# Kernel tuning notes

Hardware: AMD Instinct MI355X
Metric: run time of the kernel (lower is better)

Reference implementation:

```python
import jax, jax.numpy as jnp
import numpy as np

B, T, C = 8, 1024, 576
NH, NKV = 9, 3          # query heads, kv heads
HD = C // NH            # 64 head dim
KVC = C // NKV          # 192 kv proj width
N_REP = NH // NKV       # 3


def setup_inputs() -> dict:
    key = jax.random.key(0)
    ks = jax.random.split(key, 9)
    s = 0.02
    return {
        "x": jax.random.normal(ks[0], (B, T, C), jnp.float32),
        "Wq": jax.random.normal(ks[1], (C, C), jnp.float32) * s,
        "bq": jax.random.normal(ks[2], (C,), jnp.float32) * s,
        "Wk": jax.random.normal(ks[3], (C, KVC), jnp.float32) * s,
        "bk": jax.random.normal(ks[4], (KVC,), jnp.float32) * s,
        "Wv": jax.random.normal(ks[5], (C, KVC), jnp.float32) * s,
        "bv": jax.random.normal(ks[6], (KVC,), jnp.float32) * s,
        "Wo": jax.random.normal(ks[7], (C, C), jnp.float32) * s,
        "bo": jax.random.normal(ks[8], (C,), jnp.float32) * s,
    }


def reference(x, Wq, bq, Wk, bk, Wv, bv, Wo, bo):
    Bx, Tx, Cx = x.shape
    q = x @ Wq + bq                                # [B,T,C]
    k = x @ Wk + bk                                # [B,T,KVC]
    v = x @ Wv + bv
    # split heads: q -> [B,NH,T,HD]; k,v -> [B,NKV,T,HD]
    q = q.reshape(Bx, Tx, NH, HD).transpose(0, 2, 1, 3)
    k = k.reshape(Bx, Tx, NKV, HD).transpose(0, 2, 1, 3)
    v = v.reshape(Bx, Tx, NKV, HD).transpose(0, 2, 1, 3)
    # repeat_kv: [B,NKV,T,HD] -> [B,NKV*N_REP,T,HD]
    k = jnp.repeat(k, N_REP, axis=1)
    v = jnp.repeat(v, N_REP, axis=1)
    att = jnp.einsum("bhqd,bhkd->bhqk", q, k) * (1.0 / np.sqrt(HD))
    mask = jnp.tril(jnp.ones((Tx, Tx), bool))
    att = jnp.where(mask, att, -jnp.inf)
    att = jax.nn.softmax(att, axis=-1)
    y = jnp.einsum("bhqk,bhkd->bhqd", att, v)      # [B,NH,T,HD]
    y = y.transpose(0, 2, 1, 3).reshape(Bx, Tx, Cx)
    return y @ Wo + bo
```

## Files before the change

kernel.cpp:

```cpp
#include <hip/hip_runtime.h>
#include <hip/hip_bf16.h>
#include <math.h>

#define B_    8
#define T_    1024
#define C_    576
#define NH_   9
#define NKV_  3
#define HD_   64
#define KVC_  192
#define NREP_ 3
#define NQKV_ 960

typedef __attribute__((ext_vector_type(8))) short bf16x8;
typedef __attribute__((ext_vector_type(4))) float f32x4;
typedef __attribute__((ext_vector_type(4))) int i32x4;

#define MFMA_16x16x32(a, b, c) __builtin_amdgcn_mfma_f32_16x16x32_bf16((a), (b), (c), 0, 0, 0)

__device__ __forceinline__ ushort f2bf(float f) {
  __hip_bfloat16 h = __float2bfloat16(f);
  return *reinterpret_cast<const ushort*>(&h);
}

__device__ __forceinline__ int swz(int row, int col) {
  int byte = (row << 7) + (col << 1);
  return (byte ^ ((row & 7) << 4)) >> 1;
}

__device__ __forceinline__ i32x4 packrow(const float* src) {
  const float4 a = *reinterpret_cast<const float4*>(src);
  const float4 b = *reinterpret_cast<const float4*>(src + 4);
  union { ushort u[8]; i32x4 v; } t;
  t.u[0] = f2bf(a.x); t.u[1] = f2bf(a.y); t.u[2] = f2bf(a.z); t.u[3] = f2bf(a.w);
  t.u[4] = f2bf(b.x); t.u[5] = f2bf(b.y); t.u[6] = f2bf(b.z); t.u[7] = f2bf(b.w);
  return t.v;
}

__global__ __launch_bounds__(256) void convert_x_kernel(
    const float* __restrict__ x, ushort* __restrict__ xb) {
  const size_t idx = ((size_t)blockIdx.x * 256 + threadIdx.x) * 8;
  *reinterpret_cast<i32x4*>(xb + idx) = packrow(x + idx);
}

__global__ __launch_bounds__(256) void convert_w_kernel(
    const float* __restrict__ Wq, const float* __restrict__ Wk,
    const float* __restrict__ Wv, const float* __restrict__ Wo,
    const float* __restrict__ bq, const float* __restrict__ bk,
    const float* __restrict__ bv, const float* __restrict__ bo,
    ushort* __restrict__ wqkvT, ushort* __restrict__ woT, float* __restrict__ bcat) {
  const int n = blockIdx.x * 256 + threadIdx.x;
  const int k8 = blockIdx.y;
  const float* src; int ld; ushort* dst;
  if (n < 576)      { src = Wq + n;        ld = C_;  dst = wqkvT + (size_t)n * C_; }
  else if (n < 768) { src = Wk + (n - 576); ld = KVC_; dst = wqkvT + (size_t)n * C_; }
  else if (n < 960) { src = Wv + (n - 768); ld = KVC_; dst = wqkvT + (size_t)n * C_; }
  else              { src = Wo + (n - 960); ld = C_;  dst = woT + (size_t)(n - 960) * C_; }
  union { ushort u[8]; i32x4 v; } t;
  #pragma unroll
  for (int e = 0; e < 8; e++) t.u[e] = f2bf(src[(size_t)(k8 * 8 + e) * ld]);
  *reinterpret_cast<i32x4*>(dst + k8 * 8) = t.v;
  if (k8 == 0) {
    if (n < 576)      bcat[n] = bq[n];
    else if (n < 768) bcat[n] = bk[n - 576];
    else if (n < 960) bcat[n] = bv[n - 768];
    else              bcat[n] = bo[n - 960];
  }
}

template<bool OUT_BF16>
__global__ __launch_bounds__(256) void gemm_mfma_kernel(
    const ushort* __restrict__ A, const ushort* __restrict__ Bt,
    const float* __restrict__ bias, void* __restrict__ Cp,
    int M, int K, int N, int q_cols) {
  __shared__ ushort As[128 * 64];
  __shared__ ushort Bs[64 * 64];
  const int bm = blockIdx.y * 128, bn = blockIdx.x * 64;
  const int tid = threadIdx.x;
  const int wave = tid >> 6, lane = tid & 63;
  const int lg = lane >> 4, ll = lane & 15;
  const int wm = (wave >> 1) * 64, wn = (wave & 1) * 32;
  f32x4 acc[4][2] = {};

  for (int k0 = 0; k0 < K; k0 += 64) {
    #pragma unroll
    for (int i = 0; i < 4; i++) {
      int c = tid + i * 256;
      int row = c >> 3, colb = (c & 7) * 8;
      *reinterpret_cast<i32x4*>(&As[swz(row, colb)]) =
          *reinterpret_cast<const i32x4*>(A + (size_t)(bm + row) * K + k0 + colb);
    }
    #pragma unroll
    for (int i = 0; i < 2; i++) {
      int c = tid + i * 256;
      int row = c >> 3, colb = (c & 7) * 8;
      *reinterpret_cast<i32x4*>(&Bs[swz(row, colb)]) =
          *reinterpret_cast<const i32x4*>(Bt + (size_t)(bn + row) * K + k0 + colb);
    }
    __syncthreads();

    bf16x8 af[4][2], bfr[2][2];
    #pragma unroll
    for (int mt = 0; mt < 4; mt++) {
      af[mt][0] = *reinterpret_cast<const bf16x8*>(&As[swz(wm + mt * 16 + ll, lg * 8)]);
      af[mt][1] = *reinterpret_cast<const bf16x8*>(&As[swz(wm + mt * 16 + ll, 32 + lg * 8)]);
    }
    #pragma unroll
    for (int nt = 0; nt < 2; nt++) {
      bfr[nt][0] = *reinterpret_cast<const bf16x8*>(&Bs[swz(wn + nt * 16 + ll, lg * 8)]);
      bfr[nt][1] = *reinterpret_cast<const bf16x8*>(&Bs[swz(wn + nt * 16 + ll, 32 + lg * 8)]);
    }
    #pragma unroll
    for (int mt = 0; mt < 4; mt++) {
      #pragma unroll
      for (int nt = 0; nt < 2; nt++) {
        acc[mt][nt] = MFMA_16x16x32(af[mt][0], bfr[nt][0], acc[mt][nt]);
        acc[mt][nt] = MFMA_16x16x32(af[mt][1], bfr[nt][1], acc[mt][nt]);
      }
    }
    __syncthreads();
  }

  #pragma unroll
  for (int mt = 0; mt < 4; mt++) {
    #pragma unroll
    for (int nt = 0; nt < 2; nt++) {
      const int col = bn + wn + nt * 16 + ll;
      const float scale = (col < q_cols) ? 0.125f : 1.0f;
      #pragma unroll
      for (int r = 0; r < 4; r++) {
        const int row = bm + wm + mt * 16 + lg * 4 + r;
        const float val = (acc[mt][nt][r] + bias[col]) * scale;
        if (OUT_BF16) ((ushort*)Cp)[(size_t)row * N + col] = f2bf(val);
        else          ((float*)Cp)[(size_t)row * N + col] = val;
      }
    }
  }
}

__global__ __launch_bounds__(256) void attn_mfma_kernel(
    const ushort* __restrict__ qkv, ushort* __restrict__ y) {
  const int qt = 15 - blockIdx.z, h = blockIdx.x, b = blockIdx.y;
  const int kvh = h / NREP_;
  const int tid = threadIdx.x;
  const int wave = tid >> 6, lane = tid & 63;
  const int lg = lane >> 4, ll = lane & 15;
  const int w16 = wave << 4;
  const int qrow0 = qt << 6;
  const int nk = (qt + 2) >> 1;

  __shared__ ushort Ks[2][64 * 64];
  __shared__ ushort Vts[2][64 * 64];
  __shared__ ushort Ps[4][16 * 64];

  const int ksub = tid >> 7, ktt = tid & 127;
  const int kr = ktt >> 2, kcb = (ktt & 3) << 4;
  const int vkp = ktt & 31, vds = (ktt >> 5) << 4;

  const ushort* qrow = qkv + (size_t)(b * T_ + qrow0 + w16 + ll) * NQKV_ + h * HD_;
  const bf16x8 qa0 = *reinterpret_cast<const bf16x8*>(qrow + lg * 8);
  const bf16x8 qa1 = *reinterpret_cast<const bf16x8*>(qrow + 32 + lg * 8);

  f32x4 o[4] = {};
  float m_i = -INFINITY, l_i = 0.f;

  i32x4 kra, krb, krc, krd, va0, va1, vb0, vb1;
  {
    const size_t rb = (size_t)(b * T_);
    const ushort* ks0 = qkv + (rb + ksub * 64 + kr) * NQKV_ + 576 + kvh * HD_ + kcb;
    const ushort* ks1 = ks0 + (size_t)32 * NQKV_;
    kra = *reinterpret_cast<const i32x4*>(ks0);
    krb = *reinterpret_cast<const i32x4*>(ks0 + 8);
    krc = *reinterpret_cast<const i32x4*>(ks1);
    krd = *reinterpret_cast<const i32x4*>(ks1 + 8);
    const ushort* v0 = qkv + (rb + ksub * 64 + vkp * 2) * NQKV_ + 768 + kvh * HD_ + vds;
    const ushort* v1 = v0 + NQKV_;
    va0 = *reinterpret_cast<const i32x4*>(v0); va1 = *reinterpret_cast<const i32x4*>(v0 + 8);
    vb0 = *reinterpret_cast<const i32x4*>(v1); vb1 = *reinterpret_cast<const i32x4*>(v1 + 8);
  }
  {
    *reinterpret_cast<i32x4*>(&Ks[ksub][swz(kr, kcb)]) = kra;
    *reinterpret_cast<i32x4*>(&Ks[ksub][swz(kr, kcb + 8)]) = krb;
    *reinterpret_cast<i32x4*>(&Ks[ksub][swz(kr + 32, kcb)]) = krc;
    *reinterpret_cast<i32x4*>(&Ks[ksub][swz(kr + 32, kcb + 8)]) = krd;
    union { i32x4 v; ushort u[8]; } a0, a1, c0, c1;
    a0.v = va0; a1.v = va1; c0.v = vb0; c1.v = vb1;
    #pragma unroll
    for (int e = 0; e < 8; e++) {
      *reinterpret_cast<uint*>(&Vts[ksub][swz(vds + e, vkp * 2)]) =
          (uint)a0.u[e] | ((uint)c0.u[e] << 16);
      *reinterpret_cast<uint*>(&Vts[ksub][swz(vds + 8 + e, vkp * 2)]) =
          (uint)a1.u[e] | ((uint)c1.u[e] << 16);
    }
  }
  __syncthreads();

  #pragma unroll 1
  for (int kt = 0; kt < nk; kt++) {
    if (kt + 1 < nk) {
      const size_t rb = (size_t)(b * T_ + ((kt + 1) << 7));
      const ushort* ks0 = qkv + (rb + ksub * 64 + kr) * NQKV_ + 576 + kvh * HD_ + kcb;
      const ushort* ks1 = ks0 + (size_t)32 * NQKV_;
      kra = *reinterpret_cast<const i32x4*>(ks0);
      krb = *reinterpret_cast<const i32x4*>(ks0 + 8);
      krc = *reinterpret_cast<const i32x4*>(ks1);
      krd = *reinterpret_cast<const i32x4*>(ks1 + 8);
      const ushort* v0 = qkv + (rb + ksub * 64 + vkp * 2) * NQKV_ + 768 + kvh * HD_ + vds;
      const ushort* v1 = v0 + NQKV_;
      va0 = *reinterpret_cast<const i32x4*>(v0); va1 = *reinterpret_cast<const i32x4*>(v0 + 8);
      vb0 = *reinterpret_cast<const i32x4*>(v1); vb1 = *reinterpret_cast<const i32x4*>(v1 + 8);
    }

    f32x4 s[8];
    #pragma unroll
    for (int kc = 0; kc < 8; kc++) {
      const int sub = kc >> 2, kcl = kc & 3;
      const bf16x8 kb0 = *reinterpret_cast<const bf16x8*>(&Ks[sub][swz(kcl * 16 + ll, lg * 8)]);
      const bf16x8 kb1 = *reinterpret_cast<const bf16x8*>(&Ks[sub][swz(kcl * 16 + ll, 32 + lg * 8)]);
      f32x4 z = {};
      z = MFMA_16x16x32(kb0, qa0, z);
      s[kc] = MFMA_16x16x32(kb1, qa1, z);
    }

    if (kt == nk - 1) {
      const int qg = qrow0 + w16 + ll - (kt << 7);
      #pragma unroll
      for (int kc = 0; kc < 8; kc++)
        #pragma unroll
        for (int r = 0; r < 4; r++)
          if (kc * 16 + lg * 4 + r > qg) s[kc][r] = -INFINITY;
    }

    float t0 = s[0][0];
    #pragma unroll
    for (int kc = 0; kc < 8; kc++)
      #pragma unroll
      for (int r = 0; r < 4; r++) t0 = fmaxf(t0, s[kc][r]);
    t0 = fmaxf(t0, __shfl_xor(t0, 16));
    t0 = fmaxf(t0, __shfl_xor(t0, 32));
    if (!__all(t0 <= m_i + 8.f)) {
      const float mn = fmaxf(m_i, t0);
      const float al = __expf(m_i - mn);
      m_i = mn;
      l_i *= al;
      #pragma unroll
      for (int r = 0; r < 4; r++) {
        const float ar = __shfl(al, lg * 4 + r);
        o[0][r] *= ar; o[1][r] *= ar; o[2][r] *= ar; o[3][r] *= ar;
      }
    }

    float rs = 0.f;
    ushort* Pw = Ps[wave];
    #pragma unroll
    for (int sub = 0; sub < 2; sub++) {
      #pragma unroll
      for (int kcl = 0; kcl < 4; kcl++) {
        const int kc = sub * 4 + kcl;
        float p0 = __expf(s[kc][0] - m_i);
        float p1 = __expf(s[kc][1] - m_i);
        float p2 = __expf(s[kc][2] - m_i);
        float p3 = __expf(s[kc][3] - m_i);
        rs += (p0 + p1) + (p2 + p3);
        uint w01 = (uint)f2bf(p0) | ((uint)f2bf(p1) << 16);
        uint w23 = (uint)f2bf(p2) | ((uint)f2bf(p3) << 16);
        *reinterpret_cast<uint*>(&Pw[swz(ll, kcl * 16 + lg * 4)])     = w01;
        *reinterpret_cast<uint*>(&Pw[swz(ll, kcl * 16 + lg * 4 + 2)]) = w23;
      }
      #pragma unroll
      for (int khl = 0; khl < 2; khl++) {
        const bf16x8 pa = *reinterpret_cast<const bf16x8*>(&Pw[swz(ll, khl * 32 + lg * 8)]);
        #pragma unroll
        for (int d0 = 0; d0 < 4; d0++) {
          const bf16x8 vb = *reinterpret_cast<const bf16x8*>(&Vts[sub][swz(d0 * 16 + ll, khl * 32 + lg * 8)]);
          o[d0] = MFMA_16x16x32(pa, vb, o[d0]);
        }
      }
    }
    rs += __shfl_xor(rs, 16);
    rs += __shfl_xor(rs, 32);
    l_i += rs;

    if (kt + 1 < nk) {
      __syncthreads();
      *reinterpret_cast<i32x4*>(&Ks[ksub][swz(kr, kcb)]) = kra;
      *reinterpret_cast<i32x4*>(&Ks[ksub][swz(kr, kcb + 8)]) = krb;
      *reinterpret_cast<i32x4*>(&Ks[ksub][swz(kr + 32, kcb)]) = krc;
      *reinterpret_cast<i32x4*>(&Ks[ksub][swz(kr + 32, kcb + 8)]) = krd;
      union { i32x4 v; ushort u[8]; } a0, a1, c0, c1;
      a0.v = va0; a1.v = va1; c0.v = vb0; c1.v = vb1;
      #pragma unroll
      for (int e = 0; e < 8; e++) {
        *reinterpret_cast<uint*>(&Vts[ksub][swz(vds + e, vkp * 2)]) =
            (uint)a0.u[e] | ((uint)c0.u[e] << 16);
        *reinterpret_cast<uint*>(&Vts[ksub][swz(vds + 8 + e, vkp * 2)]) =
            (uint)a1.u[e] | ((uint)c1.u[e] << 16);
      }
      __syncthreads();
    }
  }

  #pragma unroll
  for (int r = 0; r < 4; r++) {
    const float lr = __shfl(l_i, lg * 4 + r);
    const float inv = 1.f / lr;
    ushort* yrow = y + (size_t)(b * T_ + qrow0 + w16 + lg * 4 + r) * C_ + h * HD_;
    #pragma unroll
    for (int d0 = 0; d0 < 4; d0++) {
      yrow[d0 * 16 + ll] = f2bf(o[d0][r] * inv);
    }
  }
}

extern "C" void kernel_launch(void* const* d_in, const int* in_sizes, int n_in,
                              void* d_out, int out_size, void* d_ws, size_t ws_size,
                              hipStream_t stream) {
  const float* x  = (const float*)d_in[0];
  const float* Wq = (const float*)d_in[1];
  const float* bq = (const float*)d_in[2];
  const float* Wk = (const float*)d_in[3];
  const float* bk = (const float*)d_in[4];
  const float* Wv = (const float*)d_in[5];
  const float* bv = (const float*)d_in[6];
  const float* Wo = (const float*)d_in[7];
  const float* bo = (const float*)d_in[8];
  float* out = (float*)d_out;

  const int M = B_ * T_;
  ushort* wqkvT = (ushort*)d_ws;
  ushort* woT   = wqkvT + (size_t)NQKV_ * C_;
  float*  bcat  = (float*)(woT + (size_t)C_ * C_);
  ushort* qkv   = (ushort*)(bcat + 1536);
  ushort* y     = qkv + (size_t)M * NQKV_;
  ushort* xb    = y + (size_t)M * C_;

  convert_w_kernel<<<dim3(6, 72), 256, 0, stream>>>(Wq, Wk, Wv, Wo, bq, bk, bv, bo,
                                                    wqkvT, woT, bcat);
  convert_x_kernel<<<dim3((M * C_) / (256 * 8)), 256, 0, stream>>>(x, xb);
  gemm_mfma_kernel<true><<<dim3(NQKV_ / 64, M / 128), 256, 0, stream>>>(
      xb, wqkvT, bcat, qkv, M, C_, NQKV_, 576);
  attn_mfma_kernel<<<dim3(NH_, B_, 16), 256, 0, stream>>>(qkv, y);
  gemm_mfma_kernel<false><<<dim3(C_ / 64, M / 128), 256, 0, stream>>>(
      y, woT, bcat + NQKV_, out, M, C_, C_, 0);
}
```

Before: 84.91 us.

## Double attention query tile per block and switch softmax to exp2

Each attention block now has 512 threads covering 128 query rows, not 256 threads covering 64, so every K/V tile staged in shared memory serves twice as many queries. The grid halves, and per-thread global load work for K/V staging halves. The 1/sqrt(d)*log2(e) factor is folded into the Q projection scale so the softmax can use exp2f, with the rescale threshold adjusted to match. The risks are fewer blocks for the causal load balance, worse load balance because the diagonal tile now masks a larger span, and heavier shared-memory and register pressure per block.

```diff
diff --git a/kernel.cpp b/kernel.cpp
--- a/kernel.cpp
+++ b/kernel.cpp
@@ -126,7 +126,7 @@
     #pragma unroll
     for (int nt = 0; nt < 2; nt++) {
       const int col = bn + wn + nt * 16 + ll;
-      const float scale = (col < q_cols) ? 0.125f : 1.0f;
+      const float scale = (col < q_cols) ? 0.18033688011112042f : 1.0f;
       #pragma unroll
       for (int r = 0; r < 4; r++) {
         const int row = bm + wm + mt * 16 + lg * 4 + r;
@@ -138,59 +138,52 @@
   }
 }
 
-__global__ __launch_bounds__(256) void attn_mfma_kernel(
+__global__ __launch_bounds__(512) void attn_mfma_kernel(
     const ushort* __restrict__ qkv, ushort* __restrict__ y) {
-  const int qt = 15 - blockIdx.z, h = blockIdx.x, b = blockIdx.y;
+  const int h = blockIdx.x, b = blockIdx.y;
+  const int qblk = 7 - blockIdx.z;
   const int kvh = h / NREP_;
   const int tid = threadIdx.x;
   const int wave = tid >> 6, lane = tid & 63;
   const int lg = lane >> 4, ll = lane & 15;
-  const int w16 = wave << 4;
-  const int qrow0 = qt << 6;
-  const int nk = (qt + 2) >> 1;
+  const int wtile = wave >> 2, w16 = (wave & 3) << 4;
+  const int qrow0 = qblk << 7;
+  const int nk = qblk + 1;
 
   __shared__ ushort Ks[2][64 * 64];
   __shared__ ushort Vts[2][64 * 64];
-  __shared__ ushort Ps[4][16 * 64];
-
-  const int ksub = tid >> 7, ktt = tid & 127;
-  const int kr = ktt >> 2, kcb = (ktt & 3) << 4;
-  const int vkp = ktt & 31, vds = (ktt >> 5) << 4;
-
-  const ushort* qrow = qkv + (size_t)(b * T_ + qrow0 + w16 + ll) * NQKV_ + h * HD_;
+  __shared__ ushort Ps[8][16 * 64];
+
+  const int ksub = tid >> 8, stt = tid & 255;
+  const int kr = stt >> 2, kcb = (stt & 3) << 4;
+  const int vkp = stt & 31, vds = (stt >> 5) << 3;
+
+  const int qg_row = qrow0 + wtile * 64 + w16 + ll;
+  const ushort* qrow = qkv + (size_t)(b * T_ + qg_row) * NQKV_ + h * HD_;
   const bf16x8 qa0 = *reinterpret_cast<const bf16x8*>(qrow + lg * 8);
   const bf16x8 qa1 = *reinterpret_cast<const bf16x8*>(qrow + 32 + lg * 8);
 
   f32x4 o[4] = {};
   float m_i = -INFINITY, l_i = 0.f;
 
-  i32x4 kra, krb, krc, krd, va0, va1, vb0, vb1;
+  i32x4 kra, krb, va, vb;
   {
     const size_t rb = (size_t)(b * T_);
     const ushort* ks0 = qkv + (rb + ksub * 64 + kr) * NQKV_ + 576 + kvh * HD_ + kcb;
-    const ushort* ks1 = ks0 + (size_t)32 * NQKV_;
     kra = *reinterpret_cast<const i32x4*>(ks0);
     krb = *reinterpret_cast<const i32x4*>(ks0 + 8);
-    krc = *reinterpret_cast<const i32x4*>(ks1);
-    krd = *reinterpret_cast<const i32x4*>(ks1 + 8);
     const ushort* v0 = qkv + (rb + ksub * 64 + vkp * 2) * NQKV_ + 768 + kvh * HD_ + vds;
-    const ushort* v1 = v0 + NQKV_;
-    va0 = *reinterpret_cast<const i32x4*>(v0); va1 = *reinterpret_cast<const i32x4*>(v0 + 8);
-    vb0 = *reinterpret_cast<const i32x4*>(v1); vb1 = *reinterpret_cast<const i32x4*>(v1 + 8);
+    va = *reinterpret_cast<const i32x4*>(v0);
+    vb = *reinterpret_cast<const i32x4*>(v0 + NQKV_);
   }
   {
     *reinterpret_cast<i32x4*>(&Ks[ksub][swz(kr, kcb)]) = kra;
     *reinterpret_cast<i32x4*>(&Ks[ksub][swz(kr, kcb + 8)]) = krb;
-    *reinterpret_cast<i32x4*>(&Ks[ksub][swz(kr + 32, kcb)]) = krc;
-    *reinterpret_cast<i32x4*>(&Ks[ksub][swz(kr + 32, kcb + 8)]) = krd;
-    union { i32x4 v; ushort u[8]; } a0, a1, c0, c1;
-    a0.v = va0; a1.v = va1; c0.v = vb0; c1.v = vb1;
+    union { i32x4 v; ushort u[8]; } a0, b0; a0.v = va; b0.v = vb;
     #pragma unroll
     for (int e = 0; e < 8; e++) {
       *reinterpret_cast<uint*>(&Vts[ksub][swz(vds + e, vkp * 2)]) =
-          (uint)a0.u[e] | ((uint)c0.u[e] << 16);
-      *reinterpret_cast<uint*>(&Vts[ksub][swz(vds + 8 + e, vkp * 2)]) =
-          (uint)a1.u[e] | ((uint)c1.u[e] << 16);
+          (uint)a0.u[e] | ((uint)b0.u[e] << 16);
     }
   }
   __syncthreads();
@@ -200,15 +193,11 @@
     if (kt + 1 < nk) {
       const size_t rb = (size_t)(b * T_ + ((kt + 1) << 7));
       const ushort* ks0 = qkv + (rb + ksub * 64 + kr) * NQKV_ + 576 + kvh * HD_ + kcb;
-      const ushort* ks1 = ks0 + (size_t)32 * NQKV_;
       kra = *reinterpret_cast<const i32x4*>(ks0);
       krb = *reinterpret_cast<const i32x4*>(ks0 + 8);
-      krc = *reinterpret_cast<const i32x4*>(ks1);
-      krd = *reinterpret_cast<const i32x4*>(ks1 + 8);
       const ushort* v0 = qkv + (rb + ksub * 64 + vkp * 2) * NQKV_ + 768 + kvh * HD_ + vds;
-      const ushort* v1 = v0 + NQKV_;
-      va0 = *reinterpret_cast<const i32x4*>(v0); va1 = *reinterpret_cast<const i32x4*>(v0 + 8);
-      vb0 = *reinterpret_cast<const i32x4*>(v1); vb1 = *reinterpret_cast<const i32x4*>(v1 + 8);
+      va = *reinterpret_cast<const i32x4*>(v0);
+      vb = *reinterpret_cast<const i32x4*>(v0 + NQKV_);
     }
 
     f32x4 s[8];
@@ -223,7 +212,7 @@
     }
 
     if (kt == nk - 1) {
-      const int qg = qrow0 + w16 + ll - (kt << 7);
+      const int qg = qg_row - (kt << 7);
       #pragma unroll
       for (int kc = 0; kc < 8; kc++)
         #pragma unroll
@@ -231,16 +220,17 @@
           if (kc * 16 + lg * 4 + r > qg) s[kc][r] = -INFINITY;
     }
 
-    float t0 = s[0][0];
+    float mA[8];
     #pragma unroll
     for (int kc = 0; kc < 8; kc++)
-      #pragma unroll
-      for (int r = 0; r < 4; r++) t0 = fmaxf(t0, s[kc][r]);
+      mA[kc] = fmaxf(fmaxf(s[kc][0], s[kc][1]), fmaxf(s[kc][2], s[kc][3]));
+    float t0 = fmaxf(fmaxf(fmaxf(mA[0], mA[1]), fmaxf(mA[2], mA[3])),
+                     fmaxf(fmaxf(mA[4], mA[5]), fmaxf(mA[6], mA[7])));
     t0 = fmaxf(t0, __shfl_xor(t0, 16));
     t0 = fmaxf(t0, __shfl_xor(t0, 32));
-    if (!__all(t0 <= m_i + 8.f)) {
+    if (!__all(t0 <= m_i + 11.5415603f)) {
       const float mn = fmaxf(m_i, t0);
-      const float al = __expf(m_i - mn);
+      const float al = exp2f(m_i - mn);
       m_i = mn;
       l_i *= al;
       #pragma unroll
@@ -250,33 +240,36 @@
       }
     }
 
-    float rs = 0.f;
+    float rsub[2];
     ushort* Pw = Ps[wave];
     #pragma unroll
     for (int sub = 0; sub < 2; sub++) {
+      float rk[4];
       #pragma unroll
       for (int kcl = 0; kcl < 4; kcl++) {
         const int kc = sub * 4 + kcl;
-        float p0 = __expf(s[kc][0] - m_i);
-        float p1 = __expf(s[kc][1] - m_i);
-        float p2 = __expf(s[kc][2] - m_i);
-        float p3 = __expf(s[kc][3] - m_i);
-        rs += (p0 + p1) + (p2 + p3);
+        float p0 = exp2f(s[kc][0] - m_i);
+        float p1 = exp2f(s[kc][1] - m_i);
+        float p2 = exp2f(s[kc][2] - m_i);
+        float p3 = exp2f(s[kc][3] - m_i);
+        rk[kcl] = (p0 + p1) + (p2 + p3);
         uint w01 = (uint)f2bf(p0) | ((uint)f2bf(p1) << 16);
         uint w23 = (uint)f2bf(p2) | ((uint)f2bf(p3) << 16);
         *reinterpret_cast<uint*>(&Pw[swz(ll, kcl * 16 + lg * 4)])     = w01;
         *reinterpret_cast<uint*>(&Pw[swz(ll, kcl * 16 + lg * 4 + 2)]) = w23;
       }
+      rsub[sub] = (rk[0] + rk[1]) + (rk[2] + rk[3]);
       #pragma unroll
       for (int khl = 0; khl < 2; khl++) {
         const bf16x8 pa = *reinterpret_cast<const bf16x8*>(&Pw[swz(ll, khl * 32 + lg * 8)]);
         #pragma unroll
         for (int d0 = 0; d0 < 4; d0++) {
-          const bf16x8 vb = *reinterpret_cast<const bf16x8*>(&Vts[sub][swz(d0 * 16 + ll, khl * 32 + lg * 8)]);
-          o[d0] = MFMA_16x16x32(pa, vb, o[d0]);
+          const bf16x8 vbr = *reinterpret_cast<const bf16x8*>(&Vts[sub][swz(d0 * 16 + ll, khl * 32 + lg * 8)]);
+          o[d0] = MFMA_16x16x32(pa, vbr, o[d0]);
         }
       }
     }
+    float rs = rsub[0] + rsub[1];
     rs += __shfl_xor(rs, 16);
     rs += __shfl_xor(rs, 32);
     l_i += rs;
@@ -285,16 +278,11 @@
       __syncthreads();
       *reinterpret_cast<i32x4*>(&Ks[ksub][swz(kr, kcb)]) = kra;
       *reinterpret_cast<i32x4*>(&Ks[ksub][swz(kr, kcb + 8)]) = krb;
-      *reinterpret_cast<i32x4*>(&Ks[ksub][swz(kr + 32, kcb)]) = krc;
-      *reinterpret_cast<i32x4*>(&Ks[ksub][swz(kr + 32, kcb + 8)]) = krd;
-      union { i32x4 v; ushort u[8]; } a0, a1, c0, c1;
-      a0.v = va0; a1.v = va1; c0.v = vb0; c1.v = vb1;
+      union { i32x4 v; ushort u[8]; } a0, b0; a0.v = va; b0.v = vb;
       #pragma unroll
       for (int e = 0; e < 8; e++) {
         *reinterpret_cast<uint*>(&Vts[ksub][swz(vds + e, vkp * 2)]) =
-            (uint)a0.u[e] | ((uint)c0.u[e] << 16);
-        *reinterpret_cast<uint*>(&Vts[ksub][swz(vds + 8 + e, vkp * 2)]) =
-            (uint)a1.u[e] | ((uint)c1.u[e] << 16);
+            (uint)a0.u[e] | ((uint)b0.u[e] << 16);
       }
       __syncthreads();
     }
@@ -304,7 +292,7 @@
   for (int r = 0; r < 4; r++) {
     const float lr = __shfl(l_i, lg * 4 + r);
     const float inv = 1.f / lr;
-    ushort* yrow = y + (size_t)(b * T_ + qrow0 + w16 + lg * 4 + r) * C_ + h * HD_;
+    ushort* yrow = y + (size_t)(b * T_ + qrow0 + wtile * 64 + w16 + lg * 4 + r) * C_ + h * HD_;
     #pragma unroll
     for (int d0 = 0; d0 < 4; d0++) {
       yrow[d0 * 16 + ll] = f2bf(o[d0][r] * inv);
@@ -339,7 +327,7 @@
   convert_x_kernel<<<dim3((M * C_) / (256 * 8)), 256, 0, stream>>>(x, xb);
   gemm_mfma_kernel<true><<<dim3(NQKV_ / 64, M / 128), 256, 0, stream>>>(
       xb, wqkvT, bcat, qkv, M, C_, NQKV_, 576);
-  attn_mfma_kernel<<<dim3(NH_, B_, 16), 256, 0, stream>>>(qkv, y);
+  attn_mfma_kernel<<<dim3(NH_, B_, 8), 512, 0, stream>>>(qkv, y);
   gemm_mfma_kernel<false><<<dim3(C_ / 64, M / 128), 256, 0, stream>>>(
       y, woT, bcat + NQKV_, out, M, C_, C_, 0);
 }
```

New measurement: 91.02 us. +7.2%, slower.

## Pre-tile GEMM operands in swizzled layout and load via direct global-to-LDS

Applied to the files above, without the earlier changes.

GEMM operands (x, weights and attention output) are now stored pre-tiled in the swizzled 128x64 / 64x64 LDS layout, so the GEMM can copy each tile straight into shared memory with global_load_lds instead of staging through registers. The softmax switches to exp2 by folding log2(e) into the Q scale, and the max and row-sum reductions become trees. This removes register staging and address math in the GEMM loops, at the cost of more complex producer kernels and scattered 2-byte stores in the attention epilogue. The convert_x kernel also contains a stray dst[0]=dst[0] self-assignment.

```diff
diff --git a/kernel.cpp b/kernel.cpp
--- a/kernel.cpp
+++ b/kernel.cpp
@@ -11,6 +11,7 @@
 #define KVC_  192
 #define NREP_ 3
 #define NQKV_ 960
+#define NTK_  9
 
 typedef __attribute__((ext_vector_type(8))) short bf16x8;
 typedef __attribute__((ext_vector_type(4))) float f32x4;
@@ -26,6 +27,12 @@
 __device__ __forceinline__ int swz(int row, int col) {
   int byte = (row << 7) + (col << 1);
   return (byte ^ ((row & 7) << 4)) >> 1;
+}
+
+__device__ __forceinline__ void gload16(const ushort* g, ushort* l) {
+  __builtin_amdgcn_global_load_lds(
+      (const __attribute__((address_space(1))) unsigned int*)g,
+      (__attribute__((address_space(3))) unsigned int*)l, 16, 0, 0);
 }
 
 __device__ __forceinline__ i32x4 packrow(const float* src) {
@@ -38,9 +45,17 @@
 }
 
 __global__ __launch_bounds__(256) void convert_x_kernel(
-    const float* __restrict__ x, ushort* __restrict__ xb) {
-  const size_t idx = ((size_t)blockIdx.x * 256 + threadIdx.x) * 8;
-  *reinterpret_cast<i32x4*>(xb + idx) = packrow(x + idx);
+    const float* __restrict__ x, ushort* __restrict__ xbt) {
+  const int tm = blockIdx.x, tk = blockIdx.y;
+  ushort* dst = xbt + ((size_t)tm * NTK_ + tk) * 8192;
+  #pragma unroll
+  for (int i = 0; i < 4; i++) {
+    const int c = threadIdx.x + i * 256;
+    const int row = c >> 3, colb = (c & 7) * 8;
+    dst[0] = dst[0];
+    *reinterpret_cast<i32x4*>(&dst[swz(row, colb)]) =
+        packrow(x + (size_t)(tm * 128 + row) * C_ + tk * 64 + colb);
+  }
 }
 
 __global__ __launch_bounds__(256) void convert_w_kernel(
@@ -49,30 +64,44 @@
     const float* __restrict__ bq, const float* __restrict__ bk,
     const float* __restrict__ bv, const float* __restrict__ bo,
     ushort* __restrict__ wqkvT, ushort* __restrict__ woT, float* __restrict__ bcat) {
-  const int n = blockIdx.x * 256 + threadIdx.x;
-  const int k8 = blockIdx.y;
-  const float* src; int ld; ushort* dst;
-  if (n < 576)      { src = Wq + n;        ld = C_;  dst = wqkvT + (size_t)n * C_; }
-  else if (n < 768) { src = Wk + (n - 576); ld = KVC_; dst = wqkvT + (size_t)n * C_; }
-  else if (n < 960) { src = Wv + (n - 768); ld = KVC_; dst = wqkvT + (size_t)n * C_; }
-  else              { src = Wo + (n - 960); ld = C_;  dst = woT + (size_t)(n - 960) * C_; }
-  union { ushort u[8]; i32x4 v; } t;
+  const int tnc = blockIdx.x, tk = blockIdx.y;
   #pragma unroll
-  for (int e = 0; e < 8; e++) t.u[e] = f2bf(src[(size_t)(k8 * 8 + e) * ld]);
-  *reinterpret_cast<i32x4*>(dst + k8 * 8) = t.v;
-  if (k8 == 0) {
-    if (n < 576)      bcat[n] = bq[n];
-    else if (n < 768) bcat[n] = bk[n - 576];
-    else if (n < 960) bcat[n] = bv[n - 768];
-    else              bcat[n] = bo[n - 960];
+  for (int i = 0; i < 2; i++) {
+    const int c = threadIdx.x + i * 256;
+    const int row = c >> 3, colb = (c & 7) * 8;
+    const float* src; int ld; ushort* dst; int ncol;
+    if (tnc < 15) {
+      const int n = tnc * 64 + row;
+      if (n < 576)      { src = Wq; ld = C_;  ncol = n; }
+      else if (n < 768) { src = Wk; ld = KVC_; ncol = n - 576; }
+      else              { src = Wv; ld = KVC_; ncol = n - 768; }
+      dst = wqkvT + ((size_t)tnc * NTK_ + tk) * 4096;
+    } else {
+      src = Wo; ld = C_; ncol = (tnc - 15) * 64 + row;
+      dst = woT + ((size_t)(tnc - 15) * NTK_ + tk) * 4096;
+    }
+    union { ushort u[8]; i32x4 v; } t;
+    #pragma unroll
+    for (int e = 0; e < 8; e++)
+      t.u[e] = f2bf(src[(size_t)(tk * 64 + colb + e) * ld + ncol]);
+    *reinterpret_cast<i32x4*>(&dst[swz(row, colb)]) = t.v;
+    if (tk == 0 && (c & 7) == 0) {
+      const int n = tnc * 64 + row;
+      float bv_;
+      if (n < 576)       bv_ = bq[n];
+      else if (n < 768)  bv_ = bk[n - 576];
+      else if (n < 960)  bv_ = bv[n - 768];
+      else               bv_ = bo[n - 960];
+      bcat[n] = bv_;
+    }
   }
 }
 
 template<bool OUT_BF16>
-__global__ __launch_bounds__(256) void gemm_mfma_kernel(
-    const ushort* __restrict__ A, const ushort* __restrict__ Bt,
+__global__ __launch_bounds__(256) void gemm_lds_kernel(
+    const ushort* __restrict__ At, const ushort* __restrict__ Bt,
     const float* __restrict__ bias, void* __restrict__ Cp,
-    int M, int K, int N, int q_cols) {
+    int N, int q_cols) {
   __shared__ ushort As[128 * 64];
   __shared__ ushort Bs[64 * 64];
   const int bm = blockIdx.y * 128, bn = blockIdx.x * 64;
@@ -82,20 +111,21 @@
   const int wm = (wave >> 1) * 64, wn = (wave & 1) * 32;
   f32x4 acc[4][2] = {};
 
-  for (int k0 = 0; k0 < K; k0 += 64) {
+  const ushort* abase = At + (size_t)blockIdx.y * NTK_ * 8192;
+  const ushort* bbase = Bt + (size_t)blockIdx.x * NTK_ * 4096;
+
+  for (int kt = 0; kt < NTK_; kt++) {
+    const ushort* ak = abase + (size_t)kt * 8192;
+    const ushort* bk = bbase + (size_t)kt * 4096;
     #pragma unroll
     for (int i = 0; i < 4; i++) {
-      int c = tid + i * 256;
-      int row = c >> 3, colb = (c & 7) * 8;
-      *reinterpret_cast<i32x4*>(&As[swz(row, colb)]) =
-          *reinterpret_cast<const i32x4*>(A + (size_t)(bm + row) * K + k0 + colb);
+      const int c0 = (wave << 6) + (i << 8);
+      gload16(ak + (size_t)(c0 + lane) * 8, &As[c0 * 8]);
     }
     #pragma unroll
     for (int i = 0; i < 2; i++) {
-      int c = tid + i * 256;
-      int row = c >> 3, colb = (c & 7) * 8;
-      *reinterpret_cast<i32x4*>(&Bs[swz(row, colb)]) =
-          *reinterpret_cast<const i32x4*>(Bt + (size_t)(bn + row) * K + k0 + colb);
+      const int c0 = (wave << 6) + (i << 8);
+      gload16(bk + (size_t)(c0 + lane) * 8, &Bs[c0 * 8]);
     }
     __syncthreads();
 
@@ -126,7 +156,7 @@
     #pragma unroll
     for (int nt = 0; nt < 2; nt++) {
       const int col = bn + wn + nt * 16 + ll;
-      const float scale = (col < q_cols) ? 0.125f : 1.0f;
+      const float scale = (col < q_cols) ? 0.18033688011112042f : 1.0f;
       #pragma unroll
       for (int r = 0; r < 4; r++) {
         const int row = bm + wm + mt * 16 + lg * 4 + r;
@@ -139,7 +169,7 @@
 }
 
 __global__ __launch_bounds__(256) void attn_mfma_kernel(
-    const ushort* __restrict__ qkv, ushort* __restrict__ y) {
+    const ushort* __restrict__ qkv, ushort* __restrict__ yt) {
   const int qt = 15 - blockIdx.z, h = blockIdx.x, b = blockIdx.y;
   const int kvh = h / NREP_;
   const int tid = threadIdx.x;
@@ -231,16 +261,17 @@
           if (kc * 16 + lg * 4 + r > qg) s[kc][r] = -INFINITY;
     }
 
-    float t0 = s[0][0];
+    float mA[8];
     #pragma unroll
     for (int kc = 0; kc < 8; kc++)
-      #pragma unroll
-      for (int r = 0; r < 4; r++) t0 = fmaxf(t0, s[kc][r]);
+      mA[kc] = fmaxf(fmaxf(s[kc][0], s[kc][1]), fmaxf(s[kc][2], s[kc][3]));
+    float t0 = fmaxf(fmaxf(fmaxf(mA[0], mA[1]), fmaxf(mA[2], mA[3])),
+                     fmaxf(fmaxf(mA[4], mA[5]), fmaxf(mA[6], mA[7])));
     t0 = fmaxf(t0, __shfl_xor(t0, 16));
     t0 = fmaxf(t0, __shfl_xor(t0, 32));
-    if (!__all(t0 <= m_i + 8.f)) {
+    if (!__all(t0 <= m_i + 11.5415603f)) {
       const float mn = fmaxf(m_i, t0);
-      const float al = __expf(m_i - mn);
+      const float al = exp2f(m_i - mn);
       m_i = mn;
       l_i *= al;
       #pragma unroll
@@ -250,33 +281,36 @@
       }
     }
 
-    float rs = 0.f;
+    float rsub[2];
     ushort* Pw = Ps[wave];
     #pragma unroll
     for (int sub = 0; sub < 2; sub++) {
+      float rk[4];
       #pragma unroll
       for (int kcl = 0; kcl < 4; kcl++) {
         const int kc = sub * 4 + kcl;
-        float p0 = __expf(s[kc][0] - m_i);
-        float p1 = __expf(s[kc][1] - m_i);
-        float p2 = __expf(s[kc][2] - m_i);
-        float p3 = __expf(s[kc][3] - m_i);
-        rs += (p0 + p1) + (p2 + p3);
+        float p0 = exp2f(s[kc][0] - m_i);
+        float p1 = exp2f(s[kc][1] - m_i);
+        float p2 = exp2f(s[kc][2] - m_i);
+        float p3 = exp2f(s[kc][3] - m_i);
+        rk[kcl] = (p0 + p1) + (p2 + p3);
         uint w01 = (uint)f2bf(p0) | ((uint)f2bf(p1) << 16);
         uint w23 = (uint)f2bf(p2) | ((uint)f2bf(p3) << 16);
         *reinterpret_cast<uint*>(&Pw[swz(ll, kcl * 16 + lg * 4)])     = w01;
         *reinterpret_cast<uint*>(&Pw[swz(ll, kcl * 16 + lg * 4 + 2)]) = w23;
       }
+      rsub[sub] = (rk[0] + rk[1]) + (rk[2] + rk[3]);
       #pragma unroll
       for (int khl = 0; khl < 2; khl++) {
         const bf16x8 pa = *reinterpret_cast<const bf16x8*>(&Pw[swz(ll, khl * 32 + lg * 8)]);
         #pragma unroll
         for (int d0 = 0; d0 < 4; d0++) {
-          const bf16x8 vb = *reinterpret_cast<const bf16x8*>(&Vts[sub][swz(d0 * 16 + ll, khl * 32 + lg * 8)]);
-          o[d0] = MFMA_16x16x32(pa, vb, o[d0]);
+          const bf16x8 vbr = *reinterpret_cast<const bf16x8*>(&Vts[sub][swz(d0 * 16 + ll, khl * 32 + lg * 8)]);
+          o[d0] = MFMA_16x16x32(pa, vbr, o[d0]);
         }
       }
     }
+    float rs = rsub[0] + rsub[1];
     rs += __shfl_xor(rs, 16);
     rs += __shfl_xor(rs, 32);
     l_i += rs;
@@ -304,10 +338,12 @@
   for (int r = 0; r < 4; r++) {
     const float lr = __shfl(l_i, lg * 4 + r);
     const float inv = 1.f / lr;
-    ushort* yrow = y + (size_t)(b * T_ + qrow0 + w16 + lg * 4 + r) * C_ + h * HD_;
+    const int rowg = b * T_ + qrow0 + w16 + lg * 4 + r;
+    ushort* ybase = yt + ((size_t)(rowg >> 7) * NTK_ + h) * 8192;
+    const int lrow = rowg & 127;
     #pragma unroll
     for (int d0 = 0; d0 < 4; d0++) {
-      yrow[d0 * 16 + ll] = f2bf(o[d0][r] * inv);
+      ybase[swz(lrow, d0 * 16 + ll)] = f2bf(o[d0][r] * inv);
     }
   }
 }
@@ -328,18 +364,18 @@
 
   const int M = B_ * T_;
   ushort* wqkvT = (ushort*)d_ws;
-  ushort* woT   = wqkvT + (size_t)NQKV_ * C_;
-  float*  bcat  = (float*)(woT + (size_t)C_ * C_);
+  ushort* woT   = wqkvT + (size_t)15 * NTK_ * 4096;
+  float*  bcat  = (float*)(woT + (size_t)9 * NTK_ * 4096);
   ushort* qkv   = (ushort*)(bcat + 1536);
-  ushort* y     = qkv + (size_t)M * NQKV_;
-  ushort* xb    = y + (size_t)M * C_;
-
-  convert_w_kernel<<<dim3(6, 72), 256, 0, stream>>>(Wq, Wk, Wv, Wo, bq, bk, bv, bo,
-                                                    wqkvT, woT, bcat);
-  convert_x_kernel<<<dim3((M * C_) / (256 * 8)), 256, 0, stream>>>(x, xb);
-  gemm_mfma_kernel<true><<<dim3(NQKV_ / 64, M / 128), 256, 0, stream>>>(
-      xb, wqkvT, bcat, qkv, M, C_, NQKV_, 576);
-  attn_mfma_kernel<<<dim3(NH_, B_, 16), 256, 0, stream>>>(qkv, y);
-  gemm_mfma_kernel<false><<<dim3(C_ / 64, M / 128), 256, 0, stream>>>(
-      y, woT, bcat + NQKV_, out, M, C_, C_, 0);
-}
+  ushort* yt    = qkv + (size_t)M * NQKV_;
+  ushort* xbt   = yt + (size_t)M * C_;
+
+  convert_w_kernel<<<dim3(24, NTK_), 256, 0, stream>>>(Wq, Wk, Wv, Wo, bq, bk, bv, bo,
+                                                       wqkvT, woT, bcat);
+  convert_x_kernel<<<dim3(M / 128, NTK_), 256, 0, stream>>>(x, xbt);
+  gemm_lds_kernel<true><<<dim3(NQKV_ / 64, M / 128), 256, 0, stream>>>(
+      xbt, wqkvT, bcat, qkv, NQKV_, 576);
+  attn_mfma_kernel<<<dim3(NH_, B_, 16), 256, 0, stream>>>(qkv, yt);
+  gemm_lds_kernel<false><<<dim3(C_ / 64, M / 128), 256, 0, stream>>>(
+      yt, woT, bcat + NQKV_, out, C_, 0);
+}
```

Result: slower. 87.94 us (+3.6%).
